# Performance work log

Hardware: AMD Instinct MI355X
Metric: run time of the kernel (lower is better)

The kernel has to match this reference:

```python
import jax, jax.numpy as jnp
import numpy as np

N = 50000      # total nodes
E = 800000     # total edges
G = 1000       # graphs in batch
H = 128        # in_channels == hidden_channels
L = 3          # num GCN layers
C = 6          # num classes
EPS = 1e-5     # BatchNorm eps


def setup_inputs() -> dict:
    key = jax.random.key(0)
    ks = jax.random.split(key, 8)
    x = jax.random.normal(ks[0], (N, H), jnp.float32)
    edge_index = jax.random.randint(ks[1], (2, E), 0, N)
    batch = jnp.sort(jax.random.randint(ks[2], (N,), 0, G))
    conv_w = jax.random.normal(ks[3], (L, H, H), jnp.float32) * 0.05
    conv_b = jnp.zeros((L, H), jnp.float32)
    bn_g = jnp.ones((L, H), jnp.float32)
    bn_b = jnp.zeros((L, H), jnp.float32)
    mlp_w1 = jax.random.normal(ks[4], (H, H), jnp.float32) * 0.05
    mlp_b1 = jnp.zeros((H,), jnp.float32)
    mlp_w2 = jax.random.normal(ks[5], (H, C), jnp.float32) * 0.05
    mlp_b2 = jnp.zeros((C,), jnp.float32)
    return {"x": x, "edge_index": edge_index, "batch": batch,
            "conv_w": conv_w, "conv_b": conv_b, "bn_g": bn_g, "bn_b": bn_b,
            "mlp_w1": mlp_w1, "mlp_b1": mlp_b1, "mlp_w2": mlp_w2, "mlp_b2": mlp_b2}


def reference(x, edge_index, batch, conv_w, conv_b, bn_g, bn_b, mlp_w1, mlp_b1, mlp_w2, mlp_b2):
    src, dst = edge_index[0], edge_index[1]
    # GCN symmetric norm with self-loops: deg over A+I
    deg = jax.ops.segment_sum(jnp.ones((E,), x.dtype), dst, num_segments=N) + 1.0
    dis = jax.lax.rsqrt(deg)                      # deg^{-1/2}, [N]
    edge_norm = (dis[src] * dis[dst])[:, None]    # [E,1]
    self_norm = (dis * dis)[:, None]              # [N,1] self-loop weight 1/deg

    for l in range(L):
        h = x @ conv_w[l]                                             # [N,H]
        agg = jax.ops.segment_sum(h[src] * edge_norm, dst, num_segments=N)
        h = agg + h * self_norm + conv_b[l]
        # BatchNorm (training-mode batch statistics, biased var)
        mu = jnp.mean(h, axis=0)
        var = jnp.var(h, axis=0)
        hn = (h - mu) * jax.lax.rsqrt(var + EPS)
        x = jax.nn.relu(hn * bn_g[l] + bn_b[l])   # dropout = identity (eval)

    # global mean pool per graph
    sums = jax.ops.segment_sum(x, batch, num_segments=G)              # [G,H]
    cnt = jax.ops.segment_sum(jnp.ones((N,), x.dtype), batch, num_segments=G)
    pooled = sums / jnp.maximum(cnt, 1.0)[:, None]

    h = jax.nn.relu(pooled @ mlp_w1 + mlp_b1)
    return h @ mlp_w2 + mlp_b2                                         # [G,C]
```

## Files before the change

### kernel.cpp

```cpp
#include <hip/hip_runtime.h>

#define Nn 50000
#define Ee 800000
#define Gg 1000
#define Hh 128
#define Cc 6
#define EPSf 1e-5f
#define SB 1024
#define NSB ((Nn + SB - 1) / SB)

typedef unsigned short u16;
typedef unsigned int u32;
typedef __attribute__((ext_vector_type(8))) short bf16x8;
typedef __attribute__((ext_vector_type(4))) float f32x4;

static __device__ inline u16 f2bf(float f) {
    u32 u = __float_as_uint(f);
    u32 r = (u + 0x7fffu + ((u >> 16) & 1u)) >> 16;
    return (u16)r;
}
static __device__ inline float bf_lo(u32 v) { return __uint_as_float(v << 16); }
static __device__ inline float bf_hi(u32 v) { return __uint_as_float(v & 0xffff0000u); }
static __device__ inline u32 pack2(float a, float b) {
    return ((u32)f2bf(b) << 16) | (u32)f2bf(a);
}

__global__ __launch_bounds__(256) void k_pre(const float* __restrict__ W3,
                                             u16* __restrict__ WT3,
                                             int* __restrict__ indeg,
                                             float* __restrict__ stats3) {
    int t = blockIdx.x * blockDim.x + threadIdx.x;
    if (t < Nn) indeg[t] = 0;
    if (t < 3 * 2 * Hh) stats3[t] = 0.0f;

    if (blockIdx.x < 3) {
        __shared__ u16 tbuf[Hh * 136];
        int l = blockIdx.x;
        const float* W = W3 + l * Hh * Hh;
        u16* WT = WT3 + l * Hh * Hh;
        int tid = threadIdx.x;
#pragma unroll
        for (int i = 0; i < 16; i++) {
            int v = tid + 256 * i;
            int r = v >> 5, c4 = v & 31;
            float4 d = ((const float4*)W)[v];
            u16* p = tbuf + r * 136 + c4 * 4;
            p[0] = f2bf(d.x); p[1] = f2bf(d.y); p[2] = f2bf(d.z); p[3] = f2bf(d.w);
        }
        __syncthreads();
#pragma unroll
        for (int i = 0; i < 64; i++) {
            int o = tid + 256 * i;
            int n = o >> 7, k = o & 127;
            WT[o] = tbuf[k * 136 + n];
        }
    }
}

__global__ void k_deg(const int* __restrict__ ei, int* __restrict__ indeg,
                      const float* __restrict__ X, u16* __restrict__ Xh,
                      u16* __restrict__ rank) {
    int t = blockIdx.x * blockDim.x + threadIdx.x;
    if (t < Nn * 32) {
        float4 v = ((const float4*)X)[t];
        ushort4 o;
        o.x = f2bf(v.x); o.y = f2bf(v.y); o.z = f2bf(v.z); o.w = f2bf(v.w);
        ((ushort4*)Xh)[t] = o;
    }
    if (t < Ee) {
        int r = atomicAdd(&indeg[ei[Ee + t]], 1);
        rank[t] = (u16)r;
    }
}

__global__ __launch_bounds__(256) void k_scan1(const int* __restrict__ indeg,
                                               int* __restrict__ rs,
                                               int* __restrict__ bsum,
                                               float* __restrict__ dis,
                                               const int* __restrict__ batch,
                                               int* __restrict__ gstart) {
    __shared__ int ts[256];
    int b = blockIdx.x;
    int t = threadIdx.x;
    int base = b * SB + t * 4;
    int v[4] = {0, 0, 0, 0};
#pragma unroll
    for (int j = 0; j < 4; j++) {
        int i = base + j;
        if (i < Nn) { v[j] = indeg[i]; dis[i] = rsqrtf((float)v[j] + 1.0f); }
    }
    int g = b * 256 + t;
    if (g <= Gg) {
        int lo = 0, hi = Nn;
        while (lo < hi) {
            int mid = (lo + hi) >> 1;
            if (batch[mid] < g) lo = mid + 1; else hi = mid;
        }
        gstart[g] = lo;
    }
    int tsum = v[0] + v[1] + v[2] + v[3];
    ts[t] = tsum;
    __syncthreads();
    for (int off = 1; off < 256; off <<= 1) {
        int x = (t >= off) ? ts[t - off] : 0;
        __syncthreads();
        ts[t] += x;
        __syncthreads();
    }
    int run = (t == 0) ? 0 : ts[t - 1];
    if (t == 255) bsum[b] = ts[255];
#pragma unroll
    for (int j = 0; j < 4; j++) {
        int i = base + j;
        if (i < Nn) { rs[i] = run; run += v[j]; }
    }
}

__global__ __launch_bounds__(256) void k_scan2(int* __restrict__ rs,
                                               const int* __restrict__ bsum) {
    __shared__ int lboff[NSB];
    int t = threadIdx.x;
    if (t < 64) {
        int orig = (t < NSB) ? bsum[t] : 0;
        int v = orig;
#pragma unroll
        for (int off = 1; off < 64; off <<= 1) {
            int u = __shfl_up(v, off, 64);
            if (t >= off) v += u;
        }
        if (t < NSB) lboff[t] = v - orig;
    }
    __syncthreads();
    int i = blockIdx.x * blockDim.x + t;
    if (i < Nn) rs[i] += lboff[i >> 10];
    if (blockIdx.x == 0 && t == 0) rs[Nn] = Ee;
}

__global__ void k_fill(const int* __restrict__ ei, const int* __restrict__ rs,
                       const u16* __restrict__ rank,
                       const float* __restrict__ dis, u32* __restrict__ recs) {
    int e = blockIdx.x * blockDim.x + threadIdx.x;
    if (e >= Ee) return;
    int s = ei[e];
    int d = ei[Ee + e];
    int slot = rs[d] + (int)rank[e];
    float w = dis[s] * dis[d];
    recs[slot] = ((u32)f2bf(w) << 16) | (u32)s;
}

__global__ __launch_bounds__(256) void k_gemm(const u16* __restrict__ Xin,
                                              const u16* __restrict__ WT,
                                              u16* __restrict__ Yh,
                                              const float* __restrict__ stats,
                                              const float* __restrict__ gam,
                                              const float* __restrict__ bet,
                                              int donorm) {
    __shared__ u16 wt[Hh * 136];
    __shared__ float s_scale[Hh], s_shift[Hh];
    int tid = threadIdx.x;
    if (donorm && tid < Hh) {
        float mu = stats[tid] * (1.0f / Nn);
        float var = stats[Hh + tid] * (1.0f / Nn) - mu * mu;
        float sc = rsqrtf(var + EPSf) * gam[tid];
        s_scale[tid] = sc;
        s_shift[tid] = bet[tid] - mu * sc;
    }
#pragma unroll
    for (int i = 0; i < 8; i++) {
        int v = tid + 256 * i;
        int n = v >> 4, k8 = v & 15;
        uint4 d = ((const uint4*)WT)[v];
        *((uint4*)(wt + n * 136 + k8 * 8)) = d;
    }
    __syncthreads();

    int wv = tid >> 6, lane = tid & 63;
    int m = lane & 15, q = lane >> 4;
    int row0 = blockIdx.x * 64 + wv * 16;
    int lrow = row0 + m;
    if (lrow >= Nn) lrow = Nn - 1;
    const u16* xrow = Xin + lrow * Hh + q * 8;

    f32x4 acc[8] = {};
#pragma unroll
    for (int k0 = 0; k0 < Hh; k0 += 32) {
        bf16x8 a;
        if (donorm) {
            int cb = k0 + q * 8;
            uint4 p = *(const uint4*)(xrow + k0);
            float4 sc0 = *(const float4*)(s_scale + cb);
            float4 sc1 = *(const float4*)(s_scale + cb + 4);
            float4 sh0 = *(const float4*)(s_shift + cb);
            float4 sh1 = *(const float4*)(s_shift + cb + 4);
            float f0 = fmaxf(bf_lo(p.x) * sc0.x + sh0.x, 0.0f);
            float f1 = fmaxf(bf_hi(p.x) * sc0.y + sh0.y, 0.0f);
            float f2 = fmaxf(bf_lo(p.y) * sc0.z + sh0.z, 0.0f);
            float f3 = fmaxf(bf_hi(p.y) * sc0.w + sh0.w, 0.0f);
            float f4 = fmaxf(bf_lo(p.z) * sc1.x + sh1.x, 0.0f);
            float f5 = fmaxf(bf_hi(p.z) * sc1.y + sh1.y, 0.0f);
            float f6 = fmaxf(bf_lo(p.w) * sc1.z + sh1.z, 0.0f);
            float f7 = fmaxf(bf_hi(p.w) * sc1.w + sh1.w, 0.0f);
            union { bf16x8 v; u32 u[4]; } cv;
            cv.u[0] = pack2(f0, f1);
            cv.u[1] = pack2(f2, f3);
            cv.u[2] = pack2(f4, f5);
            cv.u[3] = pack2(f6, f7);
            a = cv.v;
        } else {
            a = *(const bf16x8*)(xrow + k0);
        }
#pragma unroll
        for (int t = 0; t < 8; t++) {
            bf16x8 b = *(const bf16x8*)(wt + (t * 16 + m) * 136 + k0 + q * 8);
            acc[t] = __builtin_amdgcn_mfma_f32_16x16x32_bf16(a, b, acc[t], 0, 0, 0);
        }
    }

    int orow0 = row0 + q * 4;
#pragma unroll
    for (int t = 0; t < 8; t++) {
#pragma unroll
        for (int r = 0; r < 4; r++) {
            int rr = orow0 + r;
            if (rr < Nn) Yh[rr * Hh + t * 16 + m] = f2bf(acc[t][r]);
        }
    }
}

__global__ __launch_bounds__(256) void k_gather(const u16* __restrict__ Yh,
                                                const float* __restrict__ dis,
                                                const float* __restrict__ bias,
                                                const int* __restrict__ rs,
                                                const u32* __restrict__ recs,
                                                u16* __restrict__ Ah) {
    int node = blockIdx.x * 4 + (threadIdx.x >> 6);
    if (node >= Nn) return;
    int lane = threadIdx.x & 63;

    const u32* rows = (const u32*)Yh;
    float dn = dis[node];
    u32 hv = rows[node * 64 + lane];
    float2 bv = ((const float2*)bias)[lane];
    float sn = dn * dn;
    float2 acc;
    acc.x = bf_lo(hv) * sn + bv.x;
    acc.y = bf_hi(hv) * sn + bv.y;

    int beg = rs[node];
    int end = rs[node + 1];

    for (int base = beg; base < end; base += 64) {
        int me = base + lane;
        u32 myrec = recs[me < end ? me : end - 1];
        int cnt = end - base;
        if (cnt > 64) cnt = 64;
        for (int i0 = 0; i0 < cnt; i0 += 16) {
            u32 rec[16]; float wgt[16]; u32 val[16];
#pragma unroll
            for (int i = 0; i < 16; i++) {
                int si = i0 + i;
                int sc = si < cnt ? si : cnt - 1;
                rec[i] = __shfl(myrec, sc, 64);
                wgt[i] = (si < cnt) ? __uint_as_float(rec[i] & 0xffff0000u) : 0.0f;
            }
#pragma unroll
            for (int i = 0; i < 16; i++) val[i] = rows[(rec[i] & 0xffffu) * 64 + lane];
#pragma unroll
            for (int i = 0; i < 16; i++) {
                acc.x += bf_lo(val[i]) * wgt[i];
                acc.y += bf_hi(val[i]) * wgt[i];
            }
        }
    }
    __builtin_nontemporal_store(pack2(acc.x, acc.y), (u32*)Ah + node * 64 + lane);
}

__global__ __launch_bounds__(256) void k_stats(const u16* __restrict__ Ah,
                                               float* __restrict__ stats) {
    __shared__ float sh[4][256];
    int t = threadIdx.x;
    int jc = t & 63, ro = t >> 6;
    const u32* col = (const u32*)Ah + jc;
    float sx = 0.f, sy = 0.f, qx = 0.f, qy = 0.f;
    for (int r = blockIdx.x * 16 + ro * 4; r < Nn; r += 4096) {
        u32 v[4];
#pragma unroll
        for (int k = 0; k < 4; k++) {
            int rr = r + k;
            v[k] = (rr < Nn) ? col[rr * 64] : 0u;
        }
#pragma unroll
        for (int k = 0; k < 4; k++) {
            float a = bf_lo(v[k]), b = bf_hi(v[k]);
            sx += a; sy += b; qx += a * a; qy += b * b;
        }
    }
    sh[0][t] = sx; sh[1][t] = sy; sh[2][t] = qx; sh[3][t] = qy;
    __syncthreads();
    if (t < 64) {
        sx = sh[0][t] + sh[0][t + 64] + sh[0][t + 128] + sh[0][t + 192];
        sy = sh[1][t] + sh[1][t + 64] + sh[1][t + 128] + sh[1][t + 192];
        qx = sh[2][t] + sh[2][t + 64] + sh[2][t + 128] + sh[2][t + 192];
        qy = sh[3][t] + sh[3][t + 64] + sh[3][t + 128] + sh[3][t + 192];
        atomicAdd(&stats[2 * t], sx);
        atomicAdd(&stats[2 * t + 1], sy);
        atomicAdd(&stats[Hh + 2 * t], qx);
        atomicAdd(&stats[Hh + 2 * t + 1], qy);
    }
}

__global__ __launch_bounds__(128) void k_poolmlp(const u16* __restrict__ Ah,
                                                 const float* __restrict__ stats,
                                                 const float* __restrict__ gam,
                                                 const float* __restrict__ bet,
                                                 const int* __restrict__ gstart,
                                                 const float* __restrict__ W1,
                                                 const float* __restrict__ b1,
                                                 const float* __restrict__ W2,
                                                 const float* __restrict__ b2,
                                                 float* __restrict__ out) {
    int g = blockIdx.x;
    int c = threadIdx.x;
    __shared__ float p[Hh];
    __shared__ float hid[Hh];
    float mu = stats[c] * (1.0f / Nn);
    float var = stats[Hh + c] * (1.0f / Nn) - mu * mu;
    float sc = rsqrtf(var + EPSf) * gam[c];
    float sf = bet[c] - mu * sc;
    int s = gstart[g], e = gstart[g + 1];
    float sum0 = 0.0f, sum1 = 0.0f;
    int r = s;
    for (; r + 1 < e; r += 2) {
        float v0 = __uint_as_float((u32)Ah[r * Hh + c] << 16);
        float v1 = __uint_as_float((u32)Ah[(r + 1) * Hh + c] << 16);
        sum0 += fmaxf(v0 * sc + sf, 0.0f);
        sum1 += fmaxf(v1 * sc + sf, 0.0f);
    }
    if (r < e) {
        float v = __uint_as_float((u32)Ah[r * Hh + c] << 16);
        sum0 += fmaxf(v * sc + sf, 0.0f);
    }
    int n = e - s;
    p[c] = (sum0 + sum1) / (float)(n > 1 ? n : 1);
    __syncthreads();
    float acc = b1[c];
    for (int k = 0; k < Hh; k++) acc += p[k] * W1[k * Hh + c];
    hid[c] = fmaxf(acc, 0.0f);
    __syncthreads();
    if (c < Cc) {
        float acc2 = b2[c];
        for (int k = 0; k < Hh; k++) acc2 += hid[k] * W2[k * Cc + c];
        out[g * Cc + c] = acc2;
    }
}

extern "C" void kernel_launch(void* const* d_in, const int* in_sizes, int n_in,
                              void* d_out, int out_size, void* d_ws, size_t ws_size,
                              hipStream_t stream) {
    const float* x      = (const float*)d_in[0];
    const int*   ei     = (const int*)d_in[1];
    const int*   batch  = (const int*)d_in[2];
    const float* conv_w = (const float*)d_in[3];
    const float* conv_b = (const float*)d_in[4];
    const float* bn_g   = (const float*)d_in[5];
    const float* bn_b   = (const float*)d_in[6];
    const float* w1     = (const float*)d_in[7];
    const float* b1     = (const float*)d_in[8];
    const float* w2     = (const float*)d_in[9];
    const float* b2     = (const float*)d_in[10];
    float* out = (float*)d_out;

    u16*   Xh      = (u16*)d_ws;
    u16*   Yh      = Xh + Nn * Hh;
    u16*   Ah      = Yh + Nn * Hh;
    u16*   WT      = Ah + Nn * Hh;
    float* dis     = (float*)(WT + 3 * Hh * Hh);
    float* stats3  = dis + Nn;
    int*   indeg   = (int*)(stats3 + 3 * 2 * Hh);
    int*   rs      = indeg + Nn;
    int*   gstart  = rs + Nn + 1;
    int*   bsum    = gstart + Gg + 1;
    u32*   recs    = (u32*)(bsum + NSB);
    u16*   rank    = (u16*)(recs + Ee);

    k_pre<<<(Nn + 255) / 256, 256, 0, stream>>>(conv_w, WT, indeg, stats3);
    k_deg<<<(Nn * 32 + 255) / 256, 256, 0, stream>>>(ei, indeg, x, Xh, rank);
    k_scan1<<<NSB, 256, 0, stream>>>(indeg, rs, bsum, dis, batch, gstart);
    k_scan2<<<(Nn + 255) / 256, 256, 0, stream>>>(rs, bsum);
    k_fill<<<(Ee + 255) / 256, 256, 0, stream>>>(ei, rs, rank, dis, recs);

    for (int l = 0; l < 3; l++) {
        float* stats = stats3 + l * 2 * Hh;
        const u16* gin = (l == 0) ? Xh : Ah;
        const float* pst = (l == 0) ? stats3 : stats3 + (l - 1) * 2 * Hh;
        const float* pg  = (l == 0) ? bn_g : bn_g + (l - 1) * Hh;
        const float* pb  = (l == 0) ? bn_b : bn_b + (l - 1) * Hh;
        k_gemm<<<(Nn + 63) / 64, 256, 0, stream>>>(gin, WT + l * Hh * Hh, Yh,
                                                   pst, pg, pb, (l == 0) ? 0 : 1);
        k_gather<<<(Nn + 3) / 4, 256, 0, stream>>>(Yh, dis, conv_b + l * Hh, rs,
                                                   recs, Ah);
        k_stats<<<256, 256, 0, stream>>>(Ah, stats);
    }

    k_poolmlp<<<Gg, 128, 0, stream>>>(Ah, stats3 + 2 * 2 * Hh, bn_g + 2 * Hh,
                                      bn_b + 2 * Hh, gstart, w1, b1, w2, b2, out);
}
```

Before: 357.3 us.

## Fuse degree counting and fp32 input conversion into first-layer GEMM

Removes the separate k_deg kernel and the bf16 copy of x. The first GEMM now reads fp32 x directly and converts it to bf16 in registers, and the same launch does the in-degree atomics and edge-rank writes with int4-vectorized destination loads. This saves one launch plus a write and reread of the bf16 input. It also moves the layer-0 GEMM ahead of the CSR build and reorders the layer loop. The mode branches add some register pressure to the GEMM kernel, and the atomics now share the launch with the MFMA work.

```diff
diff --git a/kernel.cpp b/kernel.cpp
--- a/kernel.cpp
+++ b/kernel.cpp
@@ -54,22 +54,6 @@
             int n = o >> 7, k = o & 127;
             WT[o] = tbuf[k * 136 + n];
         }
-    }
-}
-
-__global__ void k_deg(const int* __restrict__ ei, int* __restrict__ indeg,
-                      const float* __restrict__ X, u16* __restrict__ Xh,
-                      u16* __restrict__ rank) {
-    int t = blockIdx.x * blockDim.x + threadIdx.x;
-    if (t < Nn * 32) {
-        float4 v = ((const float4*)X)[t];
-        ushort4 o;
-        o.x = f2bf(v.x); o.y = f2bf(v.y); o.z = f2bf(v.z); o.w = f2bf(v.w);
-        ((ushort4*)Xh)[t] = o;
-    }
-    if (t < Ee) {
-        int r = atomicAdd(&indeg[ei[Ee + t]], 1);
-        rank[t] = (u16)r;
     }
 }
 
@@ -149,16 +133,35 @@
 }
 
 __global__ __launch_bounds__(256) void k_gemm(const u16* __restrict__ Xin,
+                                              const float* __restrict__ Xf,
                                               const u16* __restrict__ WT,
                                               u16* __restrict__ Yh,
                                               const float* __restrict__ stats,
                                               const float* __restrict__ gam,
                                               const float* __restrict__ bet,
-                                              int donorm) {
+                                              int mode,
+                                              const int* __restrict__ ei,
+                                              int* __restrict__ indeg,
+                                              u16* __restrict__ rank) {
     __shared__ u16 wt[Hh * 136];
     __shared__ float s_scale[Hh], s_shift[Hh];
     int tid = threadIdx.x;
-    if (donorm && tid < Hh) {
+
+    if (mode == 2) {
+        int g = blockIdx.x * 256 + tid;
+        int e0 = g * 4;
+        if (e0 < Ee) {
+            int4 d4 = ((const int4*)(ei + Ee))[g];
+            ushort4 r4;
+            r4.x = (u16)atomicAdd(&indeg[d4.x], 1);
+            r4.y = (u16)atomicAdd(&indeg[d4.y], 1);
+            r4.z = (u16)atomicAdd(&indeg[d4.z], 1);
+            r4.w = (u16)atomicAdd(&indeg[d4.w], 1);
+            ((ushort4*)rank)[g] = r4;
+        }
+    }
+
+    if (mode == 1 && tid < Hh) {
         float mu = stats[tid] * (1.0f / Nn);
         float var = stats[Hh + tid] * (1.0f / Nn) - mu * mu;
         float sc = rsqrtf(var + EPSf) * gam[tid];
@@ -180,12 +183,13 @@
     int lrow = row0 + m;
     if (lrow >= Nn) lrow = Nn - 1;
     const u16* xrow = Xin + lrow * Hh + q * 8;
+    const float* xfrow = Xf + lrow * Hh + q * 8;
 
     f32x4 acc[8] = {};
 #pragma unroll
     for (int k0 = 0; k0 < Hh; k0 += 32) {
         bf16x8 a;
-        if (donorm) {
+        if (mode == 1) {
             int cb = k0 + q * 8;
             uint4 p = *(const uint4*)(xrow + k0);
             float4 sc0 = *(const float4*)(s_scale + cb);
@@ -205,6 +209,15 @@
             cv.u[1] = pack2(f2, f3);
             cv.u[2] = pack2(f4, f5);
             cv.u[3] = pack2(f6, f7);
+            a = cv.v;
+        } else if (mode == 2) {
+            float4 u0 = *(const float4*)(xfrow + k0);
+            float4 u1 = *(const float4*)(xfrow + k0 + 4);
+            union { bf16x8 v; u32 u[4]; } cv;
+            cv.u[0] = pack2(u0.x, u0.y);
+            cv.u[1] = pack2(u0.z, u0.w);
+            cv.u[2] = pack2(u1.x, u1.y);
+            cv.u[3] = pack2(u1.z, u1.w);
             a = cv.v;
         } else {
             a = *(const bf16x8*)(xrow + k0);
@@ -370,8 +383,7 @@
     const float* b2     = (const float*)d_in[10];
     float* out = (float*)d_out;
 
-    u16*   Xh      = (u16*)d_ws;
-    u16*   Yh      = Xh + Nn * Hh;
+    u16*   Yh      = (u16*)d_ws;
     u16*   Ah      = Yh + Nn * Hh;
     u16*   WT      = Ah + Nn * Hh;
     float* dis     = (float*)(WT + 3 * Hh * Hh);
@@ -384,22 +396,24 @@
     u16*   rank    = (u16*)(recs + Ee);
 
     k_pre<<<(Nn + 255) / 256, 256, 0, stream>>>(conv_w, WT, indeg, stats3);
-    k_deg<<<(Nn * 32 + 255) / 256, 256, 0, stream>>>(ei, indeg, x, Xh, rank);
+    k_gemm<<<(Nn + 63) / 64, 256, 0, stream>>>(nullptr, x, WT, Yh,
+                                               nullptr, nullptr, nullptr, 2,
+                                               ei, indeg, rank);
     k_scan1<<<NSB, 256, 0, stream>>>(indeg, rs, bsum, dis, batch, gstart);
     k_scan2<<<(Nn + 255) / 256, 256, 0, stream>>>(rs, bsum);
     k_fill<<<(Ee + 255) / 256, 256, 0, stream>>>(ei, rs, rank, dis, recs);
 
     for (int l = 0; l < 3; l++) {
-        float* stats = stats3 + l * 2 * Hh;
-        const u16* gin = (l == 0) ? Xh : Ah;
-        const float* pst = (l == 0) ? stats3 : stats3 + (l - 1) * 2 * Hh;
-        const float* pg  = (l == 0) ? bn_g : bn_g + (l - 1) * Hh;
-        const float* pb  = (l == 0) ? bn_b : bn_b + (l - 1) * Hh;
-        k_gemm<<<(Nn + 63) / 64, 256, 0, stream>>>(gin, WT + l * Hh * Hh, Yh,
-                                                   pst, pg, pb, (l == 0) ? 0 : 1);
         k_gather<<<(Nn + 3) / 4, 256, 0, stream>>>(Yh, dis, conv_b + l * Hh, rs,
                                                    recs, Ah);
-        k_stats<<<256, 256, 0, stream>>>(Ah, stats);
+        k_stats<<<256, 256, 0, stream>>>(Ah, stats3 + l * 2 * Hh);
+        if (l < 2) {
+            k_gemm<<<(Nn + 63) / 64, 256, 0, stream>>>(Ah, nullptr,
+                                                       WT + (l + 1) * Hh * Hh, Yh,
+                                                       stats3 + l * 2 * Hh,
+                                                       bn_g + l * Hh, bn_b + l * Hh, 1,
+                                                       nullptr, nullptr, nullptr);
+        }
     }
 
     k_poolmlp<<<Gg, 128, 0, stream>>>(Ah, stats3 + 2 * 2 * Hh, bn_g + 2 * Hh,
```

Measured after the change: 354.6 us. About the same (-0.8%).
